# Optimization experiments

Hardware: AMD Instinct MI355X
Metric: run time of the kernel (lower is better)

Reference implementation:

```python
import jax, jax.numpy as jnp
import numpy as np

B, T, N, C = 4, 16, 256, 768
H = 12
D = C // H
HID = 4 * C
SCALE = D ** -0.5
EPS = 1e-5


def _layernorm(x, g, b):
    mu = jnp.mean(x, axis=-1, keepdims=True)
    var = jnp.var(x, axis=-1, keepdims=True)
    return (x - mu) * jax.lax.rsqrt(var + EPS) * g + b


def setup_inputs() -> dict:
    key = jax.random.key(0)
    ks = jax.random.split(key, 12)
    s = 0.02
    return {
        "x": jax.random.normal(ks[0], (B, T, N, C), dtype=jnp.float32),
        "ln1s_g": jnp.ones((C,), jnp.float32), "ln1s_b": jnp.zeros((C,), jnp.float32),
        "ln1t_g": jnp.ones((C,), jnp.float32), "ln1t_b": jnp.zeros((C,), jnp.float32),
        "ln2_g": jnp.ones((C,), jnp.float32), "ln2_b": jnp.zeros((C,), jnp.float32),
        "Wqkv_s": jax.random.normal(ks[1], (C, 3 * C), jnp.float32) * s,
        "Wproj_s": jax.random.normal(ks[2], (C, C), jnp.float32) * s,
        "bproj_s": jnp.zeros((C,), jnp.float32),
        "Wqkv_t": jax.random.normal(ks[3], (C, 3 * C), jnp.float32) * s,
        "Wproj_t": jax.random.normal(ks[4], (C, C), jnp.float32) * s,
        "bproj_t": jnp.zeros((C,), jnp.float32),
        "Wfc1": jax.random.normal(ks[5], (C, HID), jnp.float32) * s,
        "bfc1": jnp.zeros((HID,), jnp.float32),
        "Wfc2": jax.random.normal(ks[6], (HID, C), jnp.float32) * s,
        "bfc2": jnp.zeros((C,), jnp.float32),
    }


def _spatial_attn(x, Wqkv, Wproj, bproj):
    b, t, n, c = x.shape
    qkv = (x @ Wqkv).reshape(b, t, n, 3, H, D)
    q, k, v = jnp.moveaxis(qkv, 3, 0)  # each (B,T,N,H,D)
    attn = jnp.einsum('btnhd,btmhd->bthnm', q, k) * SCALE
    a = jax.nn.softmax(attn, axis=-1)
    o = jnp.einsum('bthnm,btmhd->btnhd', a, v).reshape(b, t, n, c)
    return o @ Wproj + bproj


def _temporal_attn(x, Wqkv, Wproj, bproj):
    b, t, n, c = x.shape
    qkv = (x @ Wqkv).reshape(b, t, n, 3, H, D)
    q, k, v = jnp.moveaxis(qkv, 3, 0)  # each (B,T,N,H,D)
    attn = jnp.einsum('btnhd,bsnhd->bnhts', q, k) * SCALE
    causal = jnp.triu(jnp.ones((t, t), dtype=bool), k=1)  # (T,T) upper mask
    attn = jnp.where(causal, -jnp.inf, attn)
    a = jax.nn.softmax(attn, axis=-1)
    o = jnp.einsum('bnhts,bsnhd->btnhd', a, v).reshape(b, t, n, c)
    return o @ Wproj + bproj


def _mlp(x, W1, b1, W2, b2):
    h = jax.nn.gelu(x @ W1 + b1, approximate=False)
    return h @ W2 + b2


def reference(x, ln1s_g, ln1s_b, ln1t_g, ln1t_b, ln2_g, ln2_b,
              Wqkv_s, Wproj_s, bproj_s, Wqkv_t, Wproj_t, bproj_t,
              Wfc1, bfc1, Wfc2, bfc2):
    x = x + _spatial_attn(_layernorm(x, ln1s_g, ln1s_b), Wqkv_s, Wproj_s, bproj_s)
    x = x + _temporal_attn(_layernorm(x, ln1t_g, ln1t_b), Wqkv_t, Wproj_t, bproj_t)
    x = x + _mlp(_layernorm(x, ln2_g, ln2_b), Wfc1, bfc1, Wfc2, bfc2)
    return x
```

## Files before the change

kernel.cpp:

```cpp
#include <hip/hip_runtime.h>

typedef unsigned short u16;
typedef __attribute__((ext_vector_type(8))) __bf16 bf16x8;
typedef __attribute__((ext_vector_type(4))) float f32x4;
typedef __attribute__((ext_vector_type(4))) u16 u16x4;
typedef __attribute__((ext_vector_type(8))) u16 u16x8;

#define DEVI static __device__ __forceinline__

DEVI u16 f2bf(float f) {
    unsigned u = __float_as_uint(f);
    u += 0x7fffu + ((u >> 16) & 1u);
    return (u16)(u >> 16);
}
DEVI float bf2f(u16 b) { return __uint_as_float(((unsigned)b) << 16); }

DEVI float gelu_f(float v) {
    float z = fabsf(v) * 0.70710678118654752f;
    float t = 1.f / (1.f + 0.3275911f * z);
    float p = t * (0.254829592f + t * (-0.284496736f + t * (1.421413741f +
              t * (-1.453152027f + t * 1.061405429f))));
    float erfz = 1.f - p * __expf(-z * z);
    erfz = (v < 0.f) ? -erfz : erfz;
    return 0.5f * v * (1.f + erfz);
}

DEVI void gll16(const void* g, void* s) {
    __builtin_amdgcn_global_load_lds((__attribute__((address_space(1))) void*)(g),
                                     (__attribute__((address_space(3))) void*)(s),
                                     16, 0, 0);
}

__global__ __launch_bounds__(256) void wtrans(const float* __restrict__ in,
                                              u16* __restrict__ out, int K, int N) {
    __shared__ float tile[32][33];
    int t = threadIdx.x;
    int n0 = blockIdx.x * 32, k0 = blockIdx.y * 32;
    int r = t >> 3, c4 = (t & 7) << 2;
    float4 v = *(const float4*)(in + (size_t)(k0 + r) * N + n0 + c4);
    tile[r][c4 + 0] = v.x; tile[r][c4 + 1] = v.y;
    tile[r][c4 + 2] = v.z; tile[r][c4 + 3] = v.w;
    __syncthreads();
    u16x4 o;
    o.x = f2bf(tile[c4 + 0][r]);
    o.y = f2bf(tile[c4 + 1][r]);
    o.z = f2bf(tile[c4 + 2][r]);
    o.w = f2bf(tile[c4 + 3][r]);
    *(u16x4*)(out + (size_t)(n0 + r) * K + k0 + c4) = o;
}

__global__ __launch_bounds__(256) void ln_bf16(const float* __restrict__ x,
                                               const float* __restrict__ g,
                                               const float* __restrict__ b,
                                               u16* __restrict__ out) {
    int l = threadIdx.x & 63;
    size_t row = (size_t)blockIdx.x * 4 + (threadIdx.x >> 6);
    const float4* xr = (const float4*)(x + row * 768);
    float4 vv[3];
    vv[0] = xr[l]; vv[1] = xr[l + 64]; vv[2] = xr[l + 128];
    float s = 0.f, ss = 0.f;
#pragma unroll
    for (int i = 0; i < 3; ++i) {
        s  += vv[i].x + vv[i].y + vv[i].z + vv[i].w;
        ss += vv[i].x * vv[i].x + vv[i].y * vv[i].y + vv[i].z * vv[i].z + vv[i].w * vv[i].w;
    }
#pragma unroll
    for (int m = 1; m < 64; m <<= 1) { s += __shfl_xor(s, m); ss += __shfl_xor(ss, m); }
    float mean = s * (1.f / 768.f);
    float rstd = rsqrtf(ss * (1.f / 768.f) - mean * mean + 1e-5f);
    const float4* gr = (const float4*)g;
    const float4* br = (const float4*)b;
    u16* orow = out + row * 768;
#pragma unroll
    for (int i = 0; i < 3; ++i) {
        float4 gv = gr[l + i * 64], bv = br[l + i * 64];
        u16x4 o;
        o.x = f2bf((vv[i].x - mean) * rstd * gv.x + bv.x);
        o.y = f2bf((vv[i].y - mean) * rstd * gv.y + bv.y);
        o.z = f2bf((vv[i].z - mean) * rstd * gv.z + bv.z);
        o.w = f2bf((vv[i].w - mean) * rstd * gv.w + bv.w);
        *(u16x4*)(orow + l * 4 + i * 256) = o;
    }
}

#define MFMA_(a, b, c) __builtin_amdgcn_mfma_f32_16x16x32_bf16(a, b, c, 0, 0, 0)

template <int HAS_BIAS, int HAS_RES, int DO_GELU, int OUT_BF16>
__global__ __launch_bounds__(256, 2) void gemm128(const u16* __restrict__ A,
                                                  const u16* __restrict__ BT,
                                                  const float* __restrict__ bias,
                                                  const float* res, void* outp,
                                                  int M, int N, int K, int nbx) {
    __shared__ __attribute__((aligned(16))) u16 lds_a[128 * 64];
    __shared__ __attribute__((aligned(16))) u16 lds_b[128 * 64];
    const int tid = threadIdx.x, l = tid & 63, wid = tid >> 6;
    const int l15 = l & 15, lhi = l >> 4;
    const int wr = wid >> 1, wcn = wid & 1;
    const int xr = l15 & 7;
    const int nwg = gridDim.x, orig = blockIdx.x;
    const int swz = (orig & 7) * (nwg >> 3) + (orig >> 3);
    const int bx = swz % nbx, by = swz / nbx;
    const int m0 = by * 128, n0 = bx * 128;
    const int nkt = K >> 6;

    f32x4 acc[4][4];
    const f32x4 FZ = {0.f, 0.f, 0.f, 0.f};
#pragma unroll
    for (int mi = 0; mi < 4; ++mi)
#pragma unroll
        for (int ni = 0; ni < 4; ++ni) acc[mi][ni] = FZ;

    for (int kt = 0; kt < nkt; ++kt) {
#pragma unroll
        for (int it = 0; it < 4; ++it) {
            int ci = it * 256 + tid;
            int rowa = ci >> 3, sl = ci & 7;
            int slx = sl ^ (rowa & 7);
            gll16(A  + (size_t)(m0 + rowa) * K + kt * 64 + slx * 8, lds_a + ci * 8);
            gll16(BT + (size_t)(n0 + rowa) * K + kt * 64 + slx * 8, lds_b + ci * 8);
        }
        __syncthreads();
#pragma unroll
        for (int ks = 0; ks < 2; ++ks) {
            bf16x8 av[4], bv[4];
#pragma unroll
            for (int mi = 0; mi < 4; ++mi)
                av[mi] = *(const bf16x8*)&lds_a[(wr * 64 + mi * 16 + l15) * 64 +
                                                ((ks * 4 + lhi) ^ xr) * 8];
#pragma unroll
            for (int ni = 0; ni < 4; ++ni)
                bv[ni] = *(const bf16x8*)&lds_b[(wcn * 64 + ni * 16 + l15) * 64 +
                                                ((ks * 4 + lhi) ^ xr) * 8];
#pragma unroll
            for (int mi = 0; mi < 4; ++mi)
#pragma unroll
                for (int ni = 0; ni < 4; ++ni)
                    acc[mi][ni] = MFMA_(av[mi], bv[ni], acc[mi][ni]);
        }
        __syncthreads();
    }

    float* sc = (float*)&lds_a[0] + (size_t)wid * 1088;
    float bs[4];
#pragma unroll
    for (int nf = 0; nf < 4; ++nf)
        bs[nf] = HAS_BIAS ? bias[n0 + wcn * 64 + nf * 16 + l15] : 0.f;

#pragma unroll
    for (int pass = 0; pass < 4; ++pass) {
        const int mf = pass;
#pragma unroll
        for (int nf = 0; nf < 4; ++nf)
#pragma unroll
            for (int r = 0; r < 4; ++r) {
                float v = acc[mf][nf][r] + bs[nf];
                if (DO_GELU) v = gelu_f(v);
                sc[(lhi * 4 + r) * 68 + nf * 16 + l15] = v;
            }
        const int rowbase = m0 + wr * 64 + pass * 16;
        if (OUT_BF16) {
#pragma unroll
            for (int itr = 0; itr < 2; ++itr) {
                const int rr = itr * 8 + (l >> 3);
                const int c0 = (l & 7) * 8;
                float4 f0 = *(float4*)&sc[rr * 68 + c0];
                float4 f1 = *(float4*)&sc[rr * 68 + c0 + 4];
                u16x8 ov;
                ov[0] = f2bf(f0.x); ov[1] = f2bf(f0.y);
                ov[2] = f2bf(f0.z); ov[3] = f2bf(f0.w);
                ov[4] = f2bf(f1.x); ov[5] = f2bf(f1.y);
                ov[6] = f2bf(f1.z); ov[7] = f2bf(f1.w);
                *(u16x8*)((u16*)outp + (size_t)(rowbase + rr) * N + n0 + wcn * 64 + c0) = ov;
            }
        } else {
#pragma unroll
            for (int itr = 0; itr < 4; ++itr) {
                const int rr = itr * 4 + lhi;
                const int c0 = l15 * 4;
                float4 f0 = *(float4*)&sc[rr * 68 + c0];
                const size_t idx = (size_t)(rowbase + rr) * N + n0 + wcn * 64 + c0;
                if (HAS_RES) {
                    float4 rv = *(const float4*)(res + idx);
                    f0.x += rv.x; f0.y += rv.y; f0.z += rv.z; f0.w += rv.w;
                }
                *(float4*)((float*)outp + idx) = f0;
            }
        }
    }
}

__global__ __launch_bounds__(256, 2) void sattn(const u16* __restrict__ qkv,
                                                u16* __restrict__ attno) {
    __shared__ __attribute__((aligned(16))) u16 p_lds[4][16][264];
    __shared__ __attribute__((aligned(16))) u16 vt_lds[64][264];
    const int tid = threadIdx.x, l = tid & 63, w = tid >> 6;
    const int lr = l & 15, lg = l >> 4;
    const int bid = blockIdx.x;
    const int h = bid % 12;
    const size_t R0 = (size_t)(bid / 12) * 256;
    const u16* base = qkv + R0 * 2304;
    const f32x4 FZ = {0.f, 0.f, 0.f, 0.f};

    {
        const u16* vrow = base + (size_t)tid * 2304 + 1536 + h * 64;
#pragma unroll
        for (int c = 0; c < 8; ++c) {
            bf16x8 vv = *(const bf16x8*)(vrow + c * 8);
            const u16* pv = (const u16*)&vv;
#pragma unroll
            for (int e = 0; e < 8; ++e) vt_lds[c * 8 + e][tid] = pv[e];
        }
    }
    __syncthreads();

    u16* attbase = attno + R0 * 768 + h * 64;
    for (int qb = 0; qb < 4; ++qb) {
        const int qrow0 = qb * 64 + w * 16;
        f32x4 acc[16];
#pragma unroll
        for (int nt = 0; nt < 16; ++nt) acc[nt] = FZ;
        const u16* qp = base + (size_t)(qrow0 + lr) * 2304 + h * 64;
#pragma unroll
        for (int ks = 0; ks < 2; ++ks) {
            bf16x8 af = *(const bf16x8*)(qp + ks * 32 + lg * 8);
#pragma unroll
            for (int nt = 0; nt < 16; ++nt) {
                const u16* kp = base + (size_t)(nt * 16 + lr) * 2304 + 768 + h * 64 + ks * 32 + lg * 8;
                bf16x8 bfr = *(const bf16x8*)kp;
                acc[nt] = __builtin_amdgcn_mfma_f32_16x16x32_bf16(af, bfr, acc[nt], 0, 0, 0);
            }
        }
#pragma unroll
        for (int r = 0; r < 4; ++r) {
            float m = acc[0][r] * 0.125f;
#pragma unroll
            for (int nt = 0; nt < 16; ++nt) { acc[nt][r] *= 0.125f; m = fmaxf(m, acc[nt][r]); }
            m = fmaxf(m, __shfl_xor(m, 1));
            m = fmaxf(m, __shfl_xor(m, 2));
            m = fmaxf(m, __shfl_xor(m, 4));
            m = fmaxf(m, __shfl_xor(m, 8));
            float ssum = 0.f;
#pragma unroll
            for (int nt = 0; nt < 16; ++nt) {
                float e = __expf(acc[nt][r] - m);
                acc[nt][r] = e; ssum += e;
            }
            ssum += __shfl_xor(ssum, 1);
            ssum += __shfl_xor(ssum, 2);
            ssum += __shfl_xor(ssum, 4);
            ssum += __shfl_xor(ssum, 8);
            float inv = 1.f / ssum;
#pragma unroll
            for (int nt = 0; nt < 16; ++nt) acc[nt][r] *= inv;
        }
#pragma unroll
        for (int nt = 0; nt < 16; ++nt)
#pragma unroll
            for (int r = 0; r < 4; ++r)
                p_lds[w][lg * 4 + r][nt * 16 + lr] = f2bf(acc[nt][r]);
        f32x4 oacc[4];
#pragma unroll
        for (int dt = 0; dt < 4; ++dt) oacc[dt] = FZ;
#pragma unroll
        for (int ks = 0; ks < 8; ++ks) {
            bf16x8 af = *(const bf16x8*)&p_lds[w][lr][ks * 32 + lg * 8];
#pragma unroll
            for (int dt = 0; dt < 4; ++dt) {
                bf16x8 bfr = *(const bf16x8*)&vt_lds[dt * 16 + lr][ks * 32 + lg * 8];
                oacc[dt] = __builtin_amdgcn_mfma_f32_16x16x32_bf16(af, bfr, oacc[dt], 0, 0, 0);
            }
        }
#pragma unroll
        for (int dt = 0; dt < 4; ++dt)
#pragma unroll
            for (int r = 0; r < 4; ++r)
                attbase[(size_t)(qrow0 + lg * 4 + r) * 768 + dt * 16 + lr] = f2bf(oacc[dt][r]);
    }
}

__global__ __launch_bounds__(256, 4) void tattn(const u16* __restrict__ qkv,
                                                u16* __restrict__ attno) {
    __shared__ float p_lds[4][16][17];
    const int tid = threadIdx.x, l = tid & 63, wv = tid >> 6;
    const int gw = blockIdx.x * 4 + wv;
    const int h = gw % 12;
    const int bn = gw / 12;
    const int n = bn & 255, b = bn >> 8;
    const u16* base = qkv + ((size_t)(b * 16) * 256 + n) * 2304;
    const size_t tstr = (size_t)256 * 2304;
    const int tk = l & 15, g = l >> 4;

    bf16x8 kv[8];
    const u16* kp = base + (size_t)tk * tstr + 768 + h * 64;
#pragma unroll
    for (int c = 0; c < 8; ++c) kv[c] = *(const bf16x8*)(kp + c * 8);

#pragma unroll
    for (int pass = 0; pass < 4; ++pass) {
        int tq = pass * 4 + g;
        const u16* qp = base + (size_t)tq * tstr + h * 64;
        float s = 0.f;
#pragma unroll
        for (int c = 0; c < 8; ++c) {
            bf16x8 qv = *(const bf16x8*)(qp + c * 8);
#pragma unroll
            for (int e = 0; e < 8; ++e) s += (float)qv[e] * (float)kv[c][e];
        }
        s = (tk <= tq) ? s * 0.125f : -1e30f;
        float m = s;
        m = fmaxf(m, __shfl_xor(m, 1));
        m = fmaxf(m, __shfl_xor(m, 2));
        m = fmaxf(m, __shfl_xor(m, 4));
        m = fmaxf(m, __shfl_xor(m, 8));
        float p = __expf(s - m);
        float ssum = p;
        ssum += __shfl_xor(ssum, 1);
        ssum += __shfl_xor(ssum, 2);
        ssum += __shfl_xor(ssum, 4);
        ssum += __shfl_xor(ssum, 8);
        p_lds[wv][tq][tk] = p / ssum;
    }
    __syncthreads();
    float vreg[16];
#pragma unroll
    for (int t2 = 0; t2 < 16; ++t2)
        vreg[t2] = bf2f(base[(size_t)t2 * tstr + 1536 + h * 64 + l]);
    u16* ob = attno + ((size_t)(b * 16) * 256 + n) * 768 + h * 64 + l;
#pragma unroll
    for (int tq = 0; tq < 16; ++tq) {
        float o = 0.f;
#pragma unroll
        for (int t2 = 0; t2 < 16; ++t2) o += p_lds[wv][tq][t2] * vreg[t2];
        ob[(size_t)tq * 256 * 768] = f2bf(o);
    }
}

extern "C" void kernel_launch(void* const* d_in, const int* in_sizes, int n_in,
                              void* d_out, int out_size, void* d_ws, size_t ws_size,
                              hipStream_t stream) {
    (void)in_sizes; (void)n_in; (void)out_size; (void)ws_size;
    const float* x       = (const float*)d_in[0];
    const float* ln1s_g  = (const float*)d_in[1];
    const float* ln1s_b  = (const float*)d_in[2];
    const float* ln1t_g  = (const float*)d_in[3];
    const float* ln1t_b  = (const float*)d_in[4];
    const float* ln2_g   = (const float*)d_in[5];
    const float* ln2_b   = (const float*)d_in[6];
    const float* Wqkv_s  = (const float*)d_in[7];
    const float* Wproj_s = (const float*)d_in[8];
    const float* bproj_s = (const float*)d_in[9];
    const float* Wqkv_t  = (const float*)d_in[10];
    const float* Wproj_t = (const float*)d_in[11];
    const float* bproj_t = (const float*)d_in[12];
    const float* Wfc1    = (const float*)d_in[13];
    const float* bfc1    = (const float*)d_in[14];
    const float* Wfc2    = (const float*)d_in[15];
    const float* bfc2    = (const float*)d_in[16];
    float* out = (float*)d_out;

    const int M = 16384, C = 768, HID = 3072, NQKV = 2304;

    char* p = (char*)d_ws;
    auto carve = [&](size_t bytes) {
        char* r = p;
        p += (bytes + 255) & ~(size_t)255;
        return r;
    };
    u16* wqkvT_s  = (u16*)carve((size_t)NQKV * C * 2);
    u16* wprojT_s = (u16*)carve((size_t)C * C * 2);
    u16* wqkvT_t  = (u16*)carve((size_t)NQKV * C * 2);
    u16* wprojT_t = (u16*)carve((size_t)C * C * 2);
    u16* wfc1T    = (u16*)carve((size_t)HID * C * 2);
    u16* wfc2T    = (u16*)carve((size_t)C * HID * 2);
    u16* xn       = (u16*)carve((size_t)M * C * 2);
    u16* attno    = (u16*)carve((size_t)M * C * 2);
    u16* big      = (u16*)carve((size_t)M * HID * 2);

    wtrans<<<dim3(NQKV / 32, C / 32), 256, 0, stream>>>(Wqkv_s, wqkvT_s, C, NQKV);
    wtrans<<<dim3(C / 32, C / 32), 256, 0, stream>>>(Wproj_s, wprojT_s, C, C);
    wtrans<<<dim3(NQKV / 32, C / 32), 256, 0, stream>>>(Wqkv_t, wqkvT_t, C, NQKV);
    wtrans<<<dim3(C / 32, C / 32), 256, 0, stream>>>(Wproj_t, wprojT_t, C, C);
    wtrans<<<dim3(HID / 32, C / 32), 256, 0, stream>>>(Wfc1, wfc1T, C, HID);
    wtrans<<<dim3(C / 32, HID / 32), 256, 0, stream>>>(Wfc2, wfc2T, HID, C);

    ln_bf16<<<M / 4, 256, 0, stream>>>(x, ln1s_g, ln1s_b, xn);
    gemm128<0, 0, 0, 1><<<(NQKV / 128) * (M / 128), 256, 0, stream>>>(
        xn, wqkvT_s, nullptr, nullptr, big, M, NQKV, C, NQKV / 128);
    sattn<<<768, 256, 0, stream>>>(big, attno);
    gemm128<1, 1, 0, 0><<<(C / 128) * (M / 128), 256, 0, stream>>>(
        attno, wprojT_s, bproj_s, x, out, M, C, C, C / 128);

    ln_bf16<<<M / 4, 256, 0, stream>>>(out, ln1t_g, ln1t_b, xn);
    gemm128<0, 0, 0, 1><<<(NQKV / 128) * (M / 128), 256, 0, stream>>>(
        xn, wqkvT_t, nullptr, nullptr, big, M, NQKV, C, NQKV / 128);
    tattn<<<12288 / 4, 256, 0, stream>>>(big, attno);
    gemm128<1, 1, 0, 0><<<(C / 128) * (M / 128), 256, 0, stream>>>(
        attno, wprojT_t, bproj_t, out, out, M, C, C, C / 128);

    ln_bf16<<<M / 4, 256, 0, stream>>>(out, ln2_g, ln2_b, xn);
    gemm128<1, 0, 1, 1><<<(HID / 128) * (M / 128), 256, 0, stream>>>(
        xn, wfc1T, bfc1, nullptr, big, M, HID, C, HID / 128);
    gemm128<1, 1, 0, 0><<<(C / 128) * (M / 128), 256, 0, stream>>>(
        big, wfc2T, bfc2, out, out, M, C, HID, C / 128);
}
```

Before: 543.2 us.

## Store intermediate residual stream in bf16 and batch weight transposes into one launch

The residual stream between the three sublayers is now written as bf16 (into the output buffer and a scratch buffer) instead of fp32. Downstream layernorms and residual adds read bf16, which halves that traffic, and only the final projection writes fp32. The six weight-transpose launches are merged into one kernel that picks its job from the block index, cutting launch overhead. The cost is extra rounding error on the residual path, and the first residual copy is staged in the output buffer.

```diff
diff --git a/kernel.cpp b/kernel.cpp
--- a/kernel.cpp
+++ b/kernel.cpp
@@ -31,13 +31,21 @@
                                      16, 0, 0);
 }
 
-__global__ __launch_bounds__(256) void wtrans(const float* __restrict__ in,
-                                              u16* __restrict__ out, int K, int N) {
+struct WTJob { const float* in; u16* out; int K; int N; int nbx; int start; };
+struct WTJobs { WTJob j[6]; };
+
+__global__ __launch_bounds__(256) void wtrans_all(WTJobs jobs) {
     __shared__ float tile[32][33];
-    int t = threadIdx.x;
-    int n0 = blockIdx.x * 32, k0 = blockIdx.y * 32;
-    int r = t >> 3, c4 = (t & 7) << 2;
-    float4 v = *(const float4*)(in + (size_t)(k0 + r) * N + n0 + c4);
+    const int bid = blockIdx.x;
+    int ji = 0;
+#pragma unroll
+    for (int i = 1; i < 6; ++i) ji = (bid >= jobs.j[i].start) ? i : ji;
+    const WTJob J = jobs.j[ji];
+    const int tix = bid - J.start;
+    const int n0 = (tix % J.nbx) * 32, k0 = (tix / J.nbx) * 32;
+    const int t = threadIdx.x;
+    const int r = t >> 3, c4 = (t & 7) << 2;
+    float4 v = *(const float4*)(J.in + (size_t)(k0 + r) * J.N + n0 + c4);
     tile[r][c4 + 0] = v.x; tile[r][c4 + 1] = v.y;
     tile[r][c4 + 2] = v.z; tile[r][c4 + 3] = v.w;
     __syncthreads();
@@ -46,13 +54,13 @@
     o.y = f2bf(tile[c4 + 1][r]);
     o.z = f2bf(tile[c4 + 2][r]);
     o.w = f2bf(tile[c4 + 3][r]);
-    *(u16x4*)(out + (size_t)(n0 + r) * K + k0 + c4) = o;
-}
-
-__global__ __launch_bounds__(256) void ln_bf16(const float* __restrict__ x,
-                                               const float* __restrict__ g,
-                                               const float* __restrict__ b,
-                                               u16* __restrict__ out) {
+    *(u16x4*)(J.out + (size_t)(n0 + r) * J.K + k0 + c4) = o;
+}
+
+__global__ __launch_bounds__(256) void ln_f32(const float* __restrict__ x,
+                                              const float* __restrict__ g,
+                                              const float* __restrict__ b,
+                                              u16* __restrict__ out) {
     int l = threadIdx.x & 63;
     size_t row = (size_t)blockIdx.x * 4 + (threadIdx.x >> 6);
     const float4* xr = (const float4*)(x + row * 768);
@@ -83,13 +91,52 @@
     }
 }
 
+__global__ __launch_bounds__(256) void ln_b16(const u16* __restrict__ x,
+                                              const float* __restrict__ g,
+                                              const float* __restrict__ b,
+                                              u16* __restrict__ out) {
+    int l = threadIdx.x & 63;
+    size_t row = (size_t)blockIdx.x * 4 + (threadIdx.x >> 6);
+    const u16* xr = x + row * 768;
+    float4 vv[3];
+#pragma unroll
+    for (int i = 0; i < 3; ++i) {
+        u16x4 t = *(const u16x4*)(xr + l * 4 + i * 256);
+        vv[i].x = bf2f(t.x); vv[i].y = bf2f(t.y);
+        vv[i].z = bf2f(t.z); vv[i].w = bf2f(t.w);
+    }
+    float s = 0.f, ss = 0.f;
+#pragma unroll
+    for (int i = 0; i < 3; ++i) {
+        s  += vv[i].x + vv[i].y + vv[i].z + vv[i].w;
+        ss += vv[i].x * vv[i].x + vv[i].y * vv[i].y + vv[i].z * vv[i].z + vv[i].w * vv[i].w;
+    }
+#pragma unroll
+    for (int m = 1; m < 64; m <<= 1) { s += __shfl_xor(s, m); ss += __shfl_xor(ss, m); }
+    float mean = s * (1.f / 768.f);
+    float rstd = rsqrtf(ss * (1.f / 768.f) - mean * mean + 1e-5f);
+    const float4* gr = (const float4*)g;
+    const float4* br = (const float4*)b;
+    u16* orow = out + row * 768;
+#pragma unroll
+    for (int i = 0; i < 3; ++i) {
+        float4 gv = gr[l + i * 64], bv = br[l + i * 64];
+        u16x4 o;
+        o.x = f2bf((vv[i].x - mean) * rstd * gv.x + bv.x);
+        o.y = f2bf((vv[i].y - mean) * rstd * gv.y + bv.y);
+        o.z = f2bf((vv[i].z - mean) * rstd * gv.z + bv.z);
+        o.w = f2bf((vv[i].w - mean) * rstd * gv.w + bv.w);
+        *(u16x4*)(orow + l * 4 + i * 256) = o;
+    }
+}
+
 #define MFMA_(a, b, c) __builtin_amdgcn_mfma_f32_16x16x32_bf16(a, b, c, 0, 0, 0)
 
-template <int HAS_BIAS, int HAS_RES, int DO_GELU, int OUT_BF16>
+template <int HAS_BIAS, int HAS_RES, int RES_BF16, int DO_GELU, int OUT_BF16>
 __global__ __launch_bounds__(256, 2) void gemm128(const u16* __restrict__ A,
                                                   const u16* __restrict__ BT,
                                                   const float* __restrict__ bias,
-                                                  const float* res, void* outp,
+                                                  const void* res, void* outp,
                                                   int M, int N, int K, int nbx) {
     __shared__ __attribute__((aligned(16))) u16 lds_a[128 * 64];
     __shared__ __attribute__((aligned(16))) u16 lds_b[128 * 64];
@@ -165,12 +212,27 @@
                 const int c0 = (l & 7) * 8;
                 float4 f0 = *(float4*)&sc[rr * 68 + c0];
                 float4 f1 = *(float4*)&sc[rr * 68 + c0 + 4];
+                const size_t idx = (size_t)(rowbase + rr) * N + n0 + wcn * 64 + c0;
+                if (HAS_RES) {
+                    if (RES_BF16) {
+                        u16x8 rv = *(const u16x8*)((const u16*)res + idx);
+                        f0.x += bf2f(rv[0]); f0.y += bf2f(rv[1]);
+                        f0.z += bf2f(rv[2]); f0.w += bf2f(rv[3]);
+                        f1.x += bf2f(rv[4]); f1.y += bf2f(rv[5]);
+                        f1.z += bf2f(rv[6]); f1.w += bf2f(rv[7]);
+                    } else {
+                        float4 r0 = *(const float4*)((const float*)res + idx);
+                        float4 r1 = *(const float4*)((const float*)res + idx + 4);
+                        f0.x += r0.x; f0.y += r0.y; f0.z += r0.z; f0.w += r0.w;
+                        f1.x += r1.x; f1.y += r1.y; f1.z += r1.z; f1.w += r1.w;
+                    }
+                }
                 u16x8 ov;
                 ov[0] = f2bf(f0.x); ov[1] = f2bf(f0.y);
                 ov[2] = f2bf(f0.z); ov[3] = f2bf(f0.w);
                 ov[4] = f2bf(f1.x); ov[5] = f2bf(f1.y);
                 ov[6] = f2bf(f1.z); ov[7] = f2bf(f1.w);
-                *(u16x8*)((u16*)outp + (size_t)(rowbase + rr) * N + n0 + wcn * 64 + c0) = ov;
+                *(u16x8*)((u16*)outp + idx) = ov;
             }
         } else {
 #pragma unroll
@@ -180,8 +242,14 @@
                 float4 f0 = *(float4*)&sc[rr * 68 + c0];
                 const size_t idx = (size_t)(rowbase + rr) * N + n0 + wcn * 64 + c0;
                 if (HAS_RES) {
-                    float4 rv = *(const float4*)(res + idx);
-                    f0.x += rv.x; f0.y += rv.y; f0.z += rv.z; f0.w += rv.w;
+                    if (RES_BF16) {
+                        u16x4 rv = *(const u16x4*)((const u16*)res + idx);
+                        f0.x += bf2f(rv.x); f0.y += bf2f(rv.y);
+                        f0.z += bf2f(rv.z); f0.w += bf2f(rv.w);
+                    } else {
+                        float4 rv = *(const float4*)((const float*)res + idx);
+                        f0.x += rv.x; f0.y += rv.y; f0.z += rv.z; f0.w += rv.w;
+                    }
                 }
                 *(float4*)((float*)outp + idx) = f0;
             }
@@ -375,31 +443,40 @@
     u16* xn       = (u16*)carve((size_t)M * C * 2);
     u16* attno    = (u16*)carve((size_t)M * C * 2);
     u16* big      = (u16*)carve((size_t)M * HID * 2);
-
-    wtrans<<<dim3(NQKV / 32, C / 32), 256, 0, stream>>>(Wqkv_s, wqkvT_s, C, NQKV);
-    wtrans<<<dim3(C / 32, C / 32), 256, 0, stream>>>(Wproj_s, wprojT_s, C, C);
-    wtrans<<<dim3(NQKV / 32, C / 32), 256, 0, stream>>>(Wqkv_t, wqkvT_t, C, NQKV);
-    wtrans<<<dim3(C / 32, C / 32), 256, 0, stream>>>(Wproj_t, wprojT_t, C, C);
-    wtrans<<<dim3(HID / 32, C / 32), 256, 0, stream>>>(Wfc1, wfc1T, C, HID);
-    wtrans<<<dim3(C / 32, HID / 32), 256, 0, stream>>>(Wfc2, wfc2T, HID, C);
-
-    ln_bf16<<<M / 4, 256, 0, stream>>>(x, ln1s_g, ln1s_b, xn);
-    gemm128<0, 0, 0, 1><<<(NQKV / 128) * (M / 128), 256, 0, stream>>>(
+    u16* xb2      = (u16*)carve((size_t)M * C * 2);
+    u16* xb1      = (u16*)d_out;
+
+    WTJobs jobs;
+    int acc = 0;
+    auto setjob = [&](int i, const float* in, u16* o, int K, int N) {
+        jobs.j[i] = {in, o, K, N, N / 32, acc};
+        acc += (N / 32) * (K / 32);
+    };
+    setjob(0, Wqkv_s, wqkvT_s, C, NQKV);
+    setjob(1, Wproj_s, wprojT_s, C, C);
+    setjob(2, Wqkv_t, wqkvT_t, C, NQKV);
+    setjob(3, Wproj_t, wprojT_t, C, C);
+    setjob(4, Wfc1, wfc1T, C, HID);
+    setjob(5, Wfc2, wfc2T, HID, C);
+    wtrans_all<<<acc, 256, 0, stream>>>(jobs);
+
+    ln_f32<<<M / 4, 256, 0, stream>>>(x, ln1s_g, ln1s_b, xn);
+    gemm128<0, 0, 0, 0, 1><<<(NQKV / 128) * (M / 128), 256, 0, stream>>>(
         xn, wqkvT_s, nullptr, nullptr, big, M, NQKV, C, NQKV / 128);
     sattn<<<768, 256, 0, stream>>>(big, attno);
-    gemm128<1, 1, 0, 0><<<(C / 128) * (M / 128), 256, 0, stream>>>(
-        attno, wprojT_s, bproj_s, x, out, M, C, C, C / 128);
-
-    ln_bf16<<<M / 4, 256, 0, stream>>>(out, ln1t_g, ln1t_b, xn);
-    gemm128<0, 0, 0, 1><<<(NQKV / 128) * (M / 128), 256, 0, stream>>>(
+    gemm128<1, 1, 0, 0, 1><<<(C / 128) * (M / 128), 256, 0, stream>>>(
+        attno, wprojT_s, bproj_s, x, xb1, M, C, C, C / 128);
+
+    ln_b16<<<M / 4, 256, 0, stream>>>(xb1, ln1t_g, ln1t_b, xn);
+    gemm128<0, 0, 0, 0, 1><<<(NQKV / 128) * (M / 128), 256, 0, stream>>>(
         xn, wqkvT_t, nullptr, nullptr, big, M, NQKV, C, NQKV / 128);
     tattn<<<12288 / 4, 256, 0, stream>>>(big, attno);
-    gemm128<1, 1, 0, 0><<<(C / 128) * (M / 128), 256, 0, stream>>>(
-        attno, wprojT_t, bproj_t, out, out, M, C, C, C / 128);
-
-    ln_bf16<<<M / 4, 256, 0, stream>>>(out, ln2_g, ln2_b, xn);
-    gemm128<1, 0, 1, 1><<<(HID / 128) * (M / 128), 256, 0, stream>>>(
+    gemm128<1, 1, 1, 0, 1><<<(C / 128) * (M / 128), 256, 0, stream>>>(
+        attno, wprojT_t, bproj_t, xb1, xb2, M, C, C, C / 128);
+
+    ln_b16<<<M / 4, 256, 0, stream>>>(xb2, ln2_g, ln2_b, xn);
+    gemm128<1, 0, 0, 1, 1><<<(HID / 128) * (M / 128), 256, 0, stream>>>(
         xn, wfc1T, bfc1, nullptr, big, M, HID, C, HID / 128);
-    gemm128<1, 1, 0, 0><<<(C / 128) * (M / 128), 256, 0, stream>>>(
-        big, wfc2T, bfc2, out, out, M, C, HID, C / 128);
-}
+    gemm128<1, 1, 1, 0, 0><<<(C / 128) * (M / 128), 256, 0, stream>>>(
+        big, wfc2T, bfc2, xb2, out, M, C, HID, C / 128);
+}
```

After: 518.6 us. 4.5% less time.
